# Kernel tuning notes

Hardware: AMD Instinct MI355X
Metric: run time of the kernel (lower is better)

## Reference

```python
import jax, jax.numpy as jnp
import numpy as np

STRIDE = 1
PAD = 1
K = 3  # kernel size


def setup_inputs() -> dict:
    key = jax.random.key(0)
    k1, k2, k3, k4 = jax.random.split(key, 4)
    B, C, H, W, O = 4, 256, 64, 64, 256
    x = jax.random.normal(k1, (B, C, H, W), jnp.float32)
    offset = jax.random.normal(k2, (B, 2 * K * K, H, W), jnp.float32)
    mask = jax.random.uniform(k3, (B, K * K, H, W), jnp.float32)
    # kaiming-ish scale for the conv weight
    weight = jax.random.normal(k4, (O, C, K, K), jnp.float32) / np.float32(np.sqrt(C * K * K))
    return {"x": x, "offset": offset, "mask": mask, "weight": weight}


def _deform_conv2d(x, offset, mask, weight, stride=STRIDE, pad=PAD):
    """Modulated deformable conv v2 (torchvision deform_conv2d semantics)."""
    B, C, H, W = x.shape
    O, _, Kh, Kw = weight.shape
    KK = Kh * Kw
    Ho = (H + 2 * pad - Kh) // stride + 1
    Wo = (W + 2 * pad - Kw) // stride + 1

    # offset layout: [B, 2*KK, Ho, Wo], pairs are (dy, dx) per kernel tap
    off = offset.reshape(B, KK, 2, Ho, Wo)
    dy, dx = off[:, :, 0], off[:, :, 1]  # [B, KK, Ho, Wo]

    ki = (jnp.arange(KK) // Kw).astype(x.dtype)  # kernel row per tap
    kj = (jnp.arange(KK) % Kw).astype(x.dtype)   # kernel col per tap
    base_y = (jnp.arange(Ho) * stride - pad).astype(x.dtype)
    base_x = (jnp.arange(Wo) * stride - pad).astype(x.dtype)

    # sampling positions [B, KK, Ho, Wo]
    py = base_y[None, None, :, None] + ki[None, :, None, None] + dy
    px = base_x[None, None, None, :] + kj[None, :, None, None] + dx

    y0 = jnp.floor(py)
    x0 = jnp.floor(px)
    wy = py - y0  # fractional weights
    wx = px - x0
    y0i = y0.astype(jnp.int32)
    x0i = x0.astype(jnp.int32)

    x_bhwc = jnp.transpose(x, (0, 2, 3, 1))  # [B, H, W, C] for gathers
    b_idx = jnp.arange(B)[:, None, None, None]

    def gather(yi, xi):
        # zero outside the image (zero-padding bilinear sampling)
        valid = (yi >= 0) & (yi < H) & (xi >= 0) & (xi < W)
        v = x_bhwc[b_idx, jnp.clip(yi, 0, H - 1), jnp.clip(xi, 0, W - 1)]  # [B,KK,Ho,Wo,C]
        return v * valid[..., None].astype(x.dtype)

    one = jnp.asarray(1, x.dtype)
    sampled = (gather(y0i, x0i) * ((one - wy) * (one - wx))[..., None]
               + gather(y0i, x0i + 1) * ((one - wy) * wx)[..., None]
               + gather(y0i + 1, x0i) * (wy * (one - wx))[..., None]
               + gather(y0i + 1, x0i + 1) * (wy * wx)[..., None])

    sampled = sampled * mask.reshape(B, KK, Ho, Wo)[..., None]  # modulation

    # weighted accumulation == implicit GEMM over (c, kk)
    return jnp.einsum('bkhwc,ock->bohw', sampled, weight.reshape(O, C, KK))


def reference(x, offset, mask, weight):
    return _deform_conv2d(x, offset, mask, weight)
```

## Files before the change

kernel.cpp:

```cpp
#include <hip/hip_runtime.h>
#include <hip/hip_bf16.h>

#define CN 256
#define HN 64
#define WN 64
#define ON 256
#define KKN 9
#define HWN 4096
#define KDIM 2304
#define KC 288

using frag_ab = __attribute__((ext_vector_type(8))) short;
using frag_cd = __attribute__((ext_vector_type(4))) float;
using short4v = __attribute__((ext_vector_type(4))) short;
using int4v   = __attribute__((ext_vector_type(4))) int;
using float4v = __attribute__((ext_vector_type(4))) float;
using float2v = __attribute__((ext_vector_type(2))) float;
using uint2v  = __attribute__((ext_vector_type(2))) unsigned;

static __device__ inline short f2bf(float f) {
    union { float f; unsigned u; } v; v.f = f;
    unsigned r = v.u + 0x7fffu + ((v.u >> 16) & 1u);
    return (short)(r >> 16);
}

__global__ __launch_bounds__(256) void prep_kernel(const float* __restrict__ x,
                                                   const float* __restrict__ wsrc,
                                                   short* __restrict__ xb16,
                                                   short* __restrict__ wtb) {
    int bidx = blockIdx.x;
    int tid  = threadIdx.x;
    if (bidx < 1024) {
        __shared__ float tile[64][65];
        int b   = bidx >> 8;
        int rem = bidx & 255;
        int c0  = (rem >> 6) * 64;
        int p0  = (rem & 63) * 64;
        int tp = tid & 63, tc = tid >> 6;
        for (int i = 0; i < 16; ++i) {
            int c = tc + i * 4;
            tile[c][tp] = x[(b * CN + c0 + c) * HWN + p0 + tp];
        }
        __syncthreads();
        int tcc = tid & 63, tpp = tid >> 6;
        for (int i = 0; i < 16; ++i) {
            int p = tpp + i * 4;
            xb16[(b * HWN + p0 + p) * CN + c0 + tcc] = f2bf(tile[tcc][p]);
        }
    } else {
        int chunk = (bidx - 1024) * 256 + tid;
        int ob  = chunk / (KC * 64);
        int rem = chunk - ob * (KC * 64);
        int kc  = rem >> 6;
        int row = rem & 63;
        int o   = ob * 64 + row;
        int kk  = kc >> 5;
        int oct = kc & 31;
        frag_ab v;
        #pragma unroll
        for (int e = 0; e < 8; ++e)
            v[e] = f2bf(wsrc[(o * CN + oct * 8 + e) * 9 + kk]);
        *(frag_ab*)&wtb[(size_t)chunk * 8] = v;
    }
}

__global__ __launch_bounds__(1024, 4) void fused_kernel(const short* __restrict__ xb16,
                                                        const short* __restrict__ wtb,
                                                        const float* __restrict__ offs,
                                                        const float* __restrict__ maskp,
                                                        float* __restrict__ out) {
    __shared__ struct {
        union {
            short Ab[2][16640];
            float outb[64 * 257];
        } mix;
        int desc[4608];
    } sm;
    int tid  = threadIdx.x;
    int m0   = blockIdx.x * 64;
    int b    = m0 >> 12;
    int h    = (m0 >> 6) & 63;
    int wv   = __builtin_amdgcn_readfirstlane(tid >> 6);
    int lane = tid & 63;
    int q    = lane >> 4, r = lane & 15;
    int wbase = 65 * (lane >> 1) * 8 + (lane & 1) * 4;
    int lane4 = lane * 4;
    int wv4   = wv * 4;

    if (tid < 576) {
        int kk = tid >> 6;
        int m  = tid & 63;
        int p  = h * 64 + m;
        int ki = kk / 3, kj = kk - ki * 3;
        float dy = offs[(b * 18 + 2 * kk) * HWN + p];
        float dx = offs[(b * 18 + 2 * kk + 1) * HWN + p];
        float mv = maskp[(b * 9 + kk) * HWN + p];
        float py = (float)(h - 1 + ki) + dy;
        float px = (float)(m - 1 + kj) + dx;
        float y0f = floorf(py), x0f = floorf(px);
        float wy = py - y0f, wx = px - x0f;
        int y0 = (int)y0f, x0 = (int)x0f;
        int4v cb; float4v cw;
        #pragma unroll
        for (int cy = 0; cy < 2; ++cy)
            #pragma unroll
            for (int cx = 0; cx < 2; ++cx) {
                int yy = y0 + cy, xx = x0 + cx;
                bool valid = (yy >= 0 && yy < HN && xx >= 0 && xx < WN);
                int yc = min(max(yy, 0), HN - 1);
                int xc = min(max(xx, 0), WN - 1);
                cb[cy * 2 + cx] = ((b * HN + yc) * WN + xc) * CN;
                float wgt = (cy ? wy : 1.f - wy) * (cx ? wx : 1.f - wx) * mv;
                cw[cy * 2 + cx] = valid ? wgt : 0.f;
            }
        int* dd = &sm.desc[tid * 8];
        *(int4v*)dd       = cb;
        *(float4v*)(dd + 4) = cw;
    }
    __syncthreads();

    frag_cd acc[2][2];
    #pragma unroll
    for (int i = 0; i < 2; ++i)
        #pragma unroll
        for (int j = 0; j < 2; ++j)
            acc[i][j] = (frag_cd){0.f, 0.f, 0.f, 0.f};

    short4v stg[4][4];
    float4v cwc[4];

    auto prefetch = [&](int kk1) {
        #pragma unroll
        for (int i = 0; i < 4; ++i) {
            int dbase = (kk1 * 64 + wv4 + i) * 8;
            int4v cb = *(const int4v*)&sm.desc[dbase];
            cwc[i]   = *(const float4v*)&sm.desc[dbase + 4];
            #pragma unroll
            for (int c = 0; c < 4; ++c)
                stg[i][c] = *(const short4v*)&xb16[cb[c] + lane4];
        }
    };

    int wg = wv >> 3;
    int cg = wv & 7;
    int ob = cg >> 1;
    int oh = (cg & 1) * 32;
    auto ld_bf = [&](int kk, int ks, int j) {
        return *(const frag_ab*)
            &wtb[(((size_t)ob * KC + kk * 32 + ks * 4 + q) * 64
                  + oh + j * 16 + r) * 8];
    };

    prefetch(0);

    for (int kk = 0; kk < KKN; ++kk) {
        short* dst = sm.mix.Ab[kk & 1];
        frag_ab bfx[2][2];
        #pragma unroll
        for (int j = 0; j < 2; ++j) {
            bfx[0][j] = ld_bf(kk, 0, j);
            bfx[1][j] = ld_bf(kk, 1, j);
        }
        #pragma unroll
        for (int i = 0; i < 4; ++i) {
            float4v cw = cwc[i];
            short4v res;
            #pragma unroll
            for (int g = 0; g < 2; ++g) {
                float2v a = (float2v){0.f, 0.f};
                #pragma unroll
                for (int c = 0; c < 4; ++c) {
                    uint2v uv = __builtin_bit_cast(uint2v, stg[i][c]);
                    unsigned uu = uv[g];
                    float2v f;
                    f.x = __builtin_bit_cast(float, uu << 16);
                    f.y = __builtin_bit_cast(float, uu & 0xffff0000u);
                    a += f * cw[c];
                }
                __hip_bfloat162 p2 = __float22bfloat162_rn(make_float2(a.x, a.y));
                res[2 * g]     = *(short*)&p2.x;
                res[2 * g + 1] = *(short*)&p2.y;
            }
            *(short4v*)&dst[wbase + (wv4 + i) * 8] = res;
        }
        if (kk < 8) prefetch(kk + 1);
        asm volatile("s_waitcnt lgkmcnt(0)" ::: "memory");
        __builtin_amdgcn_s_barrier();
        asm volatile("" ::: "memory");
        #pragma unroll
        for (int ks = 0; ks < 8; ++ks) {
            const int cur = ks & 1;
            frag_ab af[2];
            #pragma unroll
            for (int i = 0; i < 2; ++i)
                af[i] = *(const frag_ab*)
                    &dst[(65 * (ks * 4 + q) + wg * 32 + i * 16 + r) * 8];
            __builtin_amdgcn_s_setprio(1);
            #pragma unroll
            for (int i = 0; i < 2; ++i)
                #pragma unroll
                for (int j = 0; j < 2; ++j)
                    acc[i][j] = __builtin_amdgcn_mfma_f32_16x16x32_bf16(
                        af[i], bfx[cur][j], acc[i][j], 0, 0, 0);
            __builtin_amdgcn_s_setprio(0);
            if (ks < 6) {
                #pragma unroll
                for (int j = 0; j < 2; ++j)
                    bfx[cur][j] = ld_bf(kk, ks + 2, j);
            }
        }
    }
    __syncthreads();

    #pragma unroll
    for (int i = 0; i < 2; ++i)
        #pragma unroll
        for (int j = 0; j < 2; ++j) {
            int ml = wg * 32 + i * 16 + q * 4;
            int ol = cg * 32 + j * 16 + r;
            sm.mix.outb[(ml + 0) * 257 + ol] = acc[i][j][0];
            sm.mix.outb[(ml + 1) * 257 + ol] = acc[i][j][1];
            sm.mix.outb[(ml + 2) * 257 + ol] = acc[i][j][2];
            sm.mix.outb[(ml + 3) * 257 + ol] = acc[i][j][3];
        }
    __syncthreads();
    {
        int ww = tid & 63;
        int og = tid >> 6;
        #pragma unroll
        for (int oo = 0; oo < 16; ++oo) {
            int o = oo * 16 + og;
            out[(((size_t)b * ON + o) * HN + h) * WN + ww] =
                sm.mix.outb[ww * 257 + o];
        }
    }
}

extern "C" void kernel_launch(void* const* d_in, const int* in_sizes, int n_in,
                              void* d_out, int out_size, void* d_ws, size_t ws_size,
                              hipStream_t stream) {
    const float* x      = (const float*)d_in[0];
    const float* offset = (const float*)d_in[1];
    const float* mask   = (const float*)d_in[2];
    const float* weight = (const float*)d_in[3];
    float* out = (float*)d_out;

    short* xb16 = (short*)d_ws;
    short* wtb  = (short*)((char*)d_ws + 8388608);

    hipLaunchKernelGGL(prep_kernel,  dim3(1312), dim3(256),  0, stream,
                       x, weight, xb16, wtb);
    hipLaunchKernelGGL(fused_kernel, dim3(256),  dim3(1024), 0, stream,
                       xb16, wtb, offset, mask, out);
}
```

Before: 122.1 us.

## Split waves into producer and consumer roles for gather and MFMA

Warps are specialised: waves 8-15 only gather and bilinear-blend the deformable samples into the double-buffered LDS tile, and waves 0-7 only run the MFMA GEMM over the full 64-row tile with 4x2 accumulators. The producers work one tap ahead of the consumers so that gather latency overlaps with matrix math from other waves, and the gathers are software-pipelined in pairs. In exchange, half as many waves issue the gathers, consumer waves hold twice as many accumulators, and some waves sit idle at the final epilogue.

```diff
diff --git a/kernel.cpp b/kernel.cpp
--- a/kernel.cpp
+++ b/kernel.cpp
@@ -85,7 +85,6 @@
     int q    = lane >> 4, r = lane & 15;
     int wbase = 65 * (lane >> 1) * 8 + (lane & 1) * 4;
     int lane4 = lane * 4;
-    int wv4   = wv * 4;
 
     if (tid < 576) {
         int kk = tid >> 6;
@@ -119,51 +118,24 @@
     }
     __syncthreads();
 
-    frag_cd acc[2][2];
-    #pragma unroll
-    for (int i = 0; i < 2; ++i)
-        #pragma unroll
-        for (int j = 0; j < 2; ++j)
-            acc[i][j] = (frag_cd){0.f, 0.f, 0.f, 0.f};
-
-    short4v stg[4][4];
-    float4v cwc[4];
-
-    auto prefetch = [&](int kk1) {
-        #pragma unroll
-        for (int i = 0; i < 4; ++i) {
-            int dbase = (kk1 * 64 + wv4 + i) * 8;
+    bool isP = (wv >= 8);
+    int  pw8 = (wv - 8) * 8;
+
+    auto g2 = [&](short4v (&stg)[2][4], int t, int roff) {
+        #pragma unroll
+        for (int i = 0; i < 2; ++i) {
+            int dbase = (t * 64 + pw8 + roff + i) * 8;
             int4v cb = *(const int4v*)&sm.desc[dbase];
-            cwc[i]   = *(const float4v*)&sm.desc[dbase + 4];
             #pragma unroll
             for (int c = 0; c < 4; ++c)
                 stg[i][c] = *(const short4v*)&xb16[cb[c] + lane4];
         }
     };
-
-    int wg = wv >> 3;
-    int cg = wv & 7;
-    int ob = cg >> 1;
-    int oh = (cg & 1) * 32;
-    auto ld_bf = [&](int kk, int ks, int j) {
-        return *(const frag_ab*)
-            &wtb[(((size_t)ob * KC + kk * 32 + ks * 4 + q) * 64
-                  + oh + j * 16 + r) * 8];
-    };
-
-    prefetch(0);
-
-    for (int kk = 0; kk < KKN; ++kk) {
-        short* dst = sm.mix.Ab[kk & 1];
-        frag_ab bfx[2][2];
-        #pragma unroll
-        for (int j = 0; j < 2; ++j) {
-            bfx[0][j] = ld_bf(kk, 0, j);
-            bfx[1][j] = ld_bf(kk, 1, j);
-        }
-        #pragma unroll
-        for (int i = 0; i < 4; ++i) {
-            float4v cw = cwc[i];
+    auto c2 = [&](short4v (&stg)[2][4], short* dstp, int t, int roff) {
+        #pragma unroll
+        for (int i = 0; i < 2; ++i) {
+            int mloc = pw8 + roff + i;
+            float4v cw = *(const float4v*)&sm.desc[(t * 64 + mloc) * 8 + 4];
             short4v res;
             #pragma unroll
             for (int g = 0; g < 2; ++g) {
@@ -181,23 +153,54 @@
                 res[2 * g]     = *(short*)&p2.x;
                 res[2 * g + 1] = *(short*)&p2.y;
             }
-            *(short4v*)&dst[wbase + (wv4 + i) * 8] = res;
-        }
-        if (kk < 8) prefetch(kk + 1);
-        asm volatile("s_waitcnt lgkmcnt(0)" ::: "memory");
-        __builtin_amdgcn_s_barrier();
-        asm volatile("" ::: "memory");
+            *(short4v*)&dstp[wbase + mloc * 8] = res;
+        }
+    };
+    auto produce = [&](int t) {
+        short* dstp = sm.mix.Ab[t & 1];
+        short4v sA[2][4], sB[2][4];
+        g2(sA, t, 0);
+        g2(sB, t, 2);
+        c2(sA, dstp, t, 0);
+        g2(sA, t, 4);
+        c2(sB, dstp, t, 2);
+        g2(sB, t, 6);
+        c2(sA, dstp, t, 4);
+        c2(sB, dstp, t, 6);
+    };
+
+    frag_cd acc[4][2];
+    #pragma unroll
+    for (int i = 0; i < 4; ++i)
+        #pragma unroll
+        for (int j = 0; j < 2; ++j)
+            acc[i][j] = (frag_cd){0.f, 0.f, 0.f, 0.f};
+    int ob = wv >> 1;
+    int oh = (wv & 1) * 32;
+    auto ld_bf = [&](int kk, int ks, int j) {
+        return *(const frag_ab*)
+            &wtb[(((size_t)ob * KC + kk * 32 + ks * 4 + q) * 64
+                  + oh + j * 16 + r) * 8];
+    };
+    auto consume = [&](int kk) {
+        const short* dstc = sm.mix.Ab[kk & 1];
+        frag_ab bfx[2][2];
+        #pragma unroll
+        for (int j = 0; j < 2; ++j) {
+            bfx[0][j] = ld_bf(kk, 0, j);
+            bfx[1][j] = ld_bf(kk, 1, j);
+        }
         #pragma unroll
         for (int ks = 0; ks < 8; ++ks) {
             const int cur = ks & 1;
-            frag_ab af[2];
-            #pragma unroll
-            for (int i = 0; i < 2; ++i)
+            frag_ab af[4];
+            #pragma unroll
+            for (int i = 0; i < 4; ++i)
                 af[i] = *(const frag_ab*)
-                    &dst[(65 * (ks * 4 + q) + wg * 32 + i * 16 + r) * 8];
+                    &dstc[(65 * (ks * 4 + q) + i * 16 + r) * 8];
             __builtin_amdgcn_s_setprio(1);
             #pragma unroll
-            for (int i = 0; i < 2; ++i)
+            for (int i = 0; i < 4; ++i)
                 #pragma unroll
                 for (int j = 0; j < 2; ++j)
                     acc[i][j] = __builtin_amdgcn_mfma_f32_16x16x32_bf16(
@@ -209,20 +212,37 @@
                     bfx[cur][j] = ld_bf(kk, ks + 2, j);
             }
         }
-    }
-    __syncthreads();
-
-    #pragma unroll
-    for (int i = 0; i < 2; ++i)
-        #pragma unroll
-        for (int j = 0; j < 2; ++j) {
-            int ml = wg * 32 + i * 16 + q * 4;
-            int ol = cg * 32 + j * 16 + r;
-            sm.mix.outb[(ml + 0) * 257 + ol] = acc[i][j][0];
-            sm.mix.outb[(ml + 1) * 257 + ol] = acc[i][j][1];
-            sm.mix.outb[(ml + 2) * 257 + ol] = acc[i][j][2];
-            sm.mix.outb[(ml + 3) * 257 + ol] = acc[i][j][3];
-        }
+    };
+
+    if (isP) produce(0);
+    asm volatile("s_waitcnt lgkmcnt(0)" ::: "memory");
+    __builtin_amdgcn_s_barrier();
+    asm volatile("" ::: "memory");
+
+    for (int kk = 0; kk < KKN; ++kk) {
+        if (isP) {
+            if (kk < 8) produce(kk + 1);
+        } else {
+            consume(kk);
+        }
+        asm volatile("s_waitcnt lgkmcnt(0)" ::: "memory");
+        __builtin_amdgcn_s_barrier();
+        asm volatile("" ::: "memory");
+    }
+
+    if (!isP) {
+        #pragma unroll
+        for (int i = 0; i < 4; ++i)
+            #pragma unroll
+            for (int j = 0; j < 2; ++j) {
+                int ml = i * 16 + q * 4;
+                int ol = wv * 32 + j * 16 + r;
+                sm.mix.outb[(ml + 0) * 257 + ol] = acc[i][j][0];
+                sm.mix.outb[(ml + 1) * 257 + ol] = acc[i][j][1];
+                sm.mix.outb[(ml + 2) * 257 + ol] = acc[i][j][2];
+                sm.mix.outb[(ml + 3) * 257 + ol] = acc[i][j][3];
+            }
+    }
     __syncthreads();
     {
         int ww = tid & 63;
```

After: 115.9 us, median of 2. -5.1%, faster.
